# Performance work log

Measured on AMD Instinct MI355X. Metric: run time of the kernel, lower is better.

The kernel has to match this reference:

```python
import jax, jax.numpy as jnp
import numpy as np
from jax import lax

INPUT_SIZE = 64
HIDDEN = 64
LAYERS = 8
B, T = 256, 2048


def setup_inputs() -> dict:
    key = jax.random.key(0)
    ks = jax.random.split(key, 10)
    s = 1.0 / np.sqrt(HIDDEN)  # PyTorch RNN init scale U(-1/sqrt(h), 1/sqrt(h))
    u = lambda k, shape: jax.random.uniform(k, shape, jnp.float32, -s, s)
    return {
        "x": jax.random.normal(ks[0], (B, T, INPUT_SIZE), jnp.float32),
        "h_state": jnp.zeros((LAYERS, B, HIDDEN), jnp.float32),
        "W_ih0": u(ks[1], (HIDDEN, INPUT_SIZE)),        # layer-0 input weights
        "W_ih": u(ks[2], (LAYERS - 1, HIDDEN, HIDDEN)), # layers 1..7 input weights
        "W_hh": u(ks[3], (LAYERS, HIDDEN, HIDDEN)),
        "b_ih": u(ks[4], (LAYERS, HIDDEN)),
        "b_hh": u(ks[5], (LAYERS, HIDDEN)),
        "W_out": u(ks[6], (1, HIDDEN)),
        "b_out": u(ks[7], (1,)),
    }


def reference(x, h_state, W_ih0, W_ih, W_hh, b_ih, b_hh, W_out, b_out):
    # Precompute layer-0 input projection for all timesteps (one big GEMM).
    x_proj = jnp.einsum("bti,hi->bth", x, W_ih0) + b_ih[0]  # [B,T,H]
    xt = jnp.transpose(x_proj, (1, 0, 2))  # [T,B,H]

    def step(h, x_t):
        # h: [LAYERS, B, H]; one timestep of the 8-layer tanh RNN stack
        new_h = []
        inp = None
        for l in range(LAYERS):
            if l == 0:
                pre = x_t + h[0] @ W_hh[0].T + b_hh[0]
            else:
                pre = inp @ W_ih[l - 1].T + b_ih[l] + h[l] @ W_hh[l].T + b_hh[l]
            inp = jnp.tanh(pre)
            new_h.append(inp)
        return jnp.stack(new_h), inp  # carry, top-layer output

    h_final, tops = lax.scan(step, h_state, xt)  # tops: [T,B,H]
    # Batched output projection (replaces the per-timestep Python loop)
    y = jnp.transpose(tops @ W_out.T + b_out, (1, 0, 2))  # [B,T,1]
    return (y, h_final)
```

## Files before the change

kernel.cpp:

```cpp
#include <hip/hip_runtime.h>

typedef _Float16 h2 __attribute__((ext_vector_type(2)));
typedef _Float16 h8 __attribute__((ext_vector_type(8)));
typedef __fp16   g2 __attribute__((ext_vector_type(2)));
typedef __fp16   g8 __attribute__((ext_vector_type(8)));
typedef float    f32x4 __attribute__((ext_vector_type(4)));

#define TT 2048
#define HH 64
#define NL 8
#define NB 256
#define G  16
#define NCH (TT/G)
#define NI  (NCH + NL)

#define PRP 20
#define NNS 84

union GU { g8 v; g2 p[4]; h8 h; };

#define PH_BASE(l, P) (((l)*2 + (P)) * 2048)
#define CH_OFF(j, c)  ((j)*128 + ((((c) ^ ((j)&7))) * 16))

__device__ __forceinline__ float tanh_fast(float v){
    float e = __expf(2.0f * v);
    float r = __builtin_amdgcn_rcpf(e + 1.0f);
    return fmaf(-2.0f, r, 1.0f);
}


#define INTERVAL(MM, P, XC, XN) { \
    const int mm = (MM); \
    const bool act = (unsigned)(mm - wv) < (unsigned)NCH; \
    if (wv == 0){ \
        if (mm + 1 < NCH){ \
            _Pragma("unroll") \
            for (int j = 0; j < G; ++j) \
                *(_Float16*)(BB + PH_BASE(0, 1-(P)) + j*128 + (((lane>>3)^(j&7))*16) + (lane&7)*2) = (_Float16)XC[j]; \
        } \
        if (mm + 2 < NCH){ \
            _Pragma("unroll") \
            for (int j = 0; j < G; ++j) \
                XN[j] = x[((size_t)b*TT + (size_t)(mm+2)*G + j)*HH + lane]; \
        } \
    } \
    if (wv == 7 && mm >= 8){ \
         \
        GU ha0, ha1; \
        ha0.h = *(const h8*)(BB + PH_BASE(8, P) + CH_OFF(nn, g)); \
        ha1.h = *(const h8*)(BB + PH_BASE(8, P) + CH_OFF(nn, 4+g)); \
        f32x4 ay = {0.f, 0.f, 0.f, 0.f}; \
        ay = __builtin_amdgcn_mfma_f32_16x16x32_f16(ha0.v, woutB[0].v, ay, 0, 0, 0); \
        ay = __builtin_amdgcn_mfma_f32_16x16x32_f16(ha1.v, woutB[1].v, ay, 0, 0, 0); \
        if (nn == 0){ \
            f32x4 st; \
            st[0] = ay[0] + bout; st[1] = ay[1] + bout; \
            st[2] = ay[2] + bout; st[3] = ay[3] + bout; \
            *(f32x4*)(yout + (size_t)b*TT + (size_t)(mm-8)*G + g*4) = st; \
        } \
    } \
    if (act){ \
        if (wv > 0){ \
            while (((volatile int*)prodF)[wv] < mm) __builtin_amdgcn_s_sleep(1); \
            asm volatile("" ::: "memory"); \
        } \
         \
        GU bx0, bx1; \
        bx0.h = *(const h8*)(BB + PH_BASE(wv, P) + CH_OFF(nn, g)); \
        bx1.h = *(const h8*)(BB + PH_BASE(wv, P) + CH_OFF(nn, 4+g)); \
        f32x4 xd0 = {bs[0],bs[0],bs[0],bs[0]}, xd1 = {bs[1],bs[1],bs[1],bs[1]}; \
        f32x4 xd2 = {bs[2],bs[2],bs[2],bs[2]}, xd3 = {bs[3],bs[3],bs[3],bs[3]}; \
        xd0 = __builtin_amdgcn_mfma_f32_16x16x32_f16(bx0.v, wihA[0][0].v, xd0, 0, 0, 0); \
        xd0 = __builtin_amdgcn_mfma_f32_16x16x32_f16(bx1.v, wihA[0][1].v, xd0, 0, 0, 0); \
        xd1 = __builtin_amdgcn_mfma_f32_16x16x32_f16(bx0.v, wihA[1][0].v, xd1, 0, 0, 0); \
        xd1 = __builtin_amdgcn_mfma_f32_16x16x32_f16(bx1.v, wihA[1][1].v, xd1, 0, 0, 0); \
        xd2 = __builtin_amdgcn_mfma_f32_16x16x32_f16(bx0.v, wihA[2][0].v, xd2, 0, 0, 0); \
        xd2 = __builtin_amdgcn_mfma_f32_16x16x32_f16(bx1.v, wihA[2][1].v, xd2, 0, 0, 0); \
        xd3 = __builtin_amdgcn_mfma_f32_16x16x32_f16(bx0.v, wihA[3][0].v, xd3, 0, 0, 0); \
        xd3 = __builtin_amdgcn_mfma_f32_16x16x32_f16(bx1.v, wihA[3][1].v, xd3, 0, 0, 0); \
         \
        asm volatile("" ::: "memory"); \
        ((volatile int*)consF)[wv] = mm; \
         \
        *(f32x4*)(preTf + (size_t)(wv*16+nn)*NNS + 0*PRP + g*4) = xd0; \
        *(f32x4*)(preTf + (size_t)(wv*16+nn)*NNS + 1*PRP + g*4) = xd1; \
        *(f32x4*)(preTf + (size_t)(wv*16+nn)*NNS + 2*PRP + g*4) = xd2; \
        *(f32x4*)(preTf + (size_t)(wv*16+nn)*NNS + 3*PRP + g*4) = xd3; \
        f32x4 prv0, prv1, prv2, prv3; \
        { \
            const float* pb = preTf + (size_t)(wv*16+nn)*NNS + g*PRP; \
            prv0 = *(const f32x4*)(pb);      prv1 = *(const f32x4*)(pb + 4); \
            prv2 = *(const f32x4*)(pb + 8);  prv3 = *(const f32x4*)(pb + 12); \
        } \
         \
        if (wv < 7){ \
            while (((volatile int*)consF)[wv+1] < mm-1) __builtin_amdgcn_s_sleep(1); \
            asm volatile("" ::: "memory"); \
        } \
         \
        _Pragma("unroll") \
        for (int j = 0; j < G; ++j){ \
            GU hA0, hA1; \
            if (j == 0){ hA0 = hp0; hA1 = hp1; } \
            else { \
                hA0.h = *(const h8*)(BB + PH_BASE(wv+1, 1-(P)) + CH_OFF(j-1, g)); \
                hA1.h = *(const h8*)(BB + PH_BASE(wv+1, 1-(P)) + CH_OFF(j-1, 4+g)); \
            } \
            const f32x4 zz = {0.f, 0.f, 0.f, 0.f}; \
            f32x4 a00 = __builtin_amdgcn_mfma_f32_16x16x32_f16(hA0.v, whhB[0][0].v, zz, 0, 0, 0); \
            f32x4 a01 = __builtin_amdgcn_mfma_f32_16x16x32_f16(hA1.v, whhB[0][1].v, zz, 0, 0, 0); \
            f32x4 a10 = __builtin_amdgcn_mfma_f32_16x16x32_f16(hA0.v, whhB[1][0].v, zz, 0, 0, 0); \
            f32x4 a11 = __builtin_amdgcn_mfma_f32_16x16x32_f16(hA1.v, whhB[1][1].v, zz, 0, 0, 0); \
            f32x4 a20 = __builtin_amdgcn_mfma_f32_16x16x32_f16(hA0.v, whhB[2][0].v, zz, 0, 0, 0); \
            f32x4 a21 = __builtin_amdgcn_mfma_f32_16x16x32_f16(hA1.v, whhB[2][1].v, zz, 0, 0, 0); \
            f32x4 a30 = __builtin_amdgcn_mfma_f32_16x16x32_f16(hA0.v, whhB[3][0].v, zz, 0, 0, 0); \
            f32x4 a31 = __builtin_amdgcn_mfma_f32_16x16x32_f16(hA1.v, whhB[3][1].v, zz, 0, 0, 0); \
            const float s0 = a00[0] + a01[0], s1 = a10[0] + a11[0]; \
            const float s2 = a20[0] + a21[0], s3 = a30[0] + a31[0]; \
            const float pa = (g & 2) ? ((g & 1) ? s3 : s2) : ((g & 1) ? s1 : s0); \
            const float prj = (j < 4) ? prv0[j&3] : (j < 8) ? prv1[j&3] \
                             : (j < 12) ? prv2[j&3] : prv3[j&3]; \
            const float hn = tanh_fast(pa + prj); \
            *(_Float16*)(BB + PH_BASE(wv+1, 1-(P)) + j*128 + (((lane>>3)^(j&7))*16) + (lane&7)*2) = (_Float16)hn; \
            if (j == G-1){ \
                hp0.h = *(const h8*)(BB + PH_BASE(wv+1, 1-(P)) + CH_OFF(G-1, g)); \
                hp1.h = *(const h8*)(BB + PH_BASE(wv+1, 1-(P)) + CH_OFF(G-1, 4+g)); \
            } \
            if (mm - wv == NCH-1 && j == G-1) \
                hout[((size_t)wv*NB + b)*HH + lane] = hn; \
        } \
         \
        asm volatile("" ::: "memory"); \
        ((volatile int*)prodF)[wv+1] = mm + 1; \
    } \
}

__global__ void __launch_bounds__(512) rnn_kernel(
    const float* __restrict__ x,
    const float* __restrict__ h_state,
    const float* __restrict__ W_ih0,
    const float* __restrict__ W_ih,
    const float* __restrict__ W_hh,
    const float* __restrict__ b_ih,
    const float* __restrict__ b_hh,
    const float* __restrict__ W_out,
    const float* __restrict__ b_out,
    float* __restrict__ out)
{
    __shared__ __attribute__((aligned(16))) _Float16 buf[(NL+1)*2*G*HH];
    __shared__ __attribute__((aligned(16))) float preT[NL*16*NNS];
    __shared__ int prodF[16];
    __shared__ int consF[16];
    char* BB = (char*)buf;
    float* preTf = preT;
    const int tid  = threadIdx.x;
    const int wv   = tid >> 6;
    const int lane = tid & 63;
    const int g    = lane >> 4;
    const int nn   = lane & 15;
    const size_t b = blockIdx.x;

    GU wihA[4][2], whhB[4][2];
    const float* Wi = (wv == 0) ? W_ih0 : (W_ih + (size_t)(wv-1)*HH*HH);
    const float* Wh = W_hh + (size_t)wv*HH*HH;
    #pragma unroll
    for (int t = 0; t < 4; ++t){
        #pragma unroll
        for (int kt = 0; kt < 2; ++kt){
            const float* pi = Wi + (size_t)(t*16 + nn)*HH + kt*32 + g*8;
            const float* ph = Wh + (size_t)(t*16 + nn)*HH + kt*32 + g*8;
            f32x4 i0 = *(const f32x4*)(pi), i1 = *(const f32x4*)(pi + 4);
            f32x4 h0 = *(const f32x4*)(ph), h1 = *(const f32x4*)(ph + 4);
            wihA[t][kt].p[0] = __builtin_amdgcn_cvt_pkrtz(i0[0], i0[1]);
            wihA[t][kt].p[1] = __builtin_amdgcn_cvt_pkrtz(i0[2], i0[3]);
            wihA[t][kt].p[2] = __builtin_amdgcn_cvt_pkrtz(i1[0], i1[1]);
            wihA[t][kt].p[3] = __builtin_amdgcn_cvt_pkrtz(i1[2], i1[3]);
            whhB[t][kt].p[0] = __builtin_amdgcn_cvt_pkrtz(h0[0], h0[1]);
            whhB[t][kt].p[1] = __builtin_amdgcn_cvt_pkrtz(h0[2], h0[3]);
            whhB[t][kt].p[2] = __builtin_amdgcn_cvt_pkrtz(h1[0], h1[1]);
            whhB[t][kt].p[3] = __builtin_amdgcn_cvt_pkrtz(h1[2], h1[3]);
        }
    }
    float bs[4];
    #pragma unroll
    for (int t = 0; t < 4; ++t)
        bs[t] = b_ih[wv*HH + t*16 + nn] + b_hh[wv*HH + t*16 + nn];
    float bout = b_out[0];

    GU woutB[2];
    if (wv == 7){
        #pragma unroll
        for (int kt = 0; kt < 2; ++kt)
            #pragma unroll
            for (int q = 0; q < 4; ++q)
                woutB[kt].p[q] = __builtin_amdgcn_cvt_pkrtz(
                    W_out[kt*32 + g*8 + q*2], W_out[kt*32 + g*8 + q*2 + 1]);
    }

    for (int i = tid; i < (NL+1)*2*G*HH; i += 512) buf[i] = (_Float16)0.f;
    if (tid < 16){
        prodF[tid] = 0;
        consF[tid] = tid - 2;
    }
    __syncthreads();
    *(_Float16*)(BB + PH_BASE(wv+1, 1-(wv&1)) + (G-1)*128 + (((lane>>3)^((G-1)&7))*16) + (lane&7)*2)
        = (_Float16)h_state[((size_t)wv*NB + b)*HH + lane];
    float xa[G], xb[G];
    if (wv == 0){
        #pragma unroll
        for (int j = 0; j < G; ++j){
            *(_Float16*)(BB + PH_BASE(0, 1) + j*128 + (((lane>>3)^(j&7))*16) + (lane&7)*2)
                = (_Float16)x[((size_t)b*TT + j)*HH + lane];
            xa[j] = x[((size_t)b*TT + G + j)*HH + lane];
        }
    }
    __syncthreads();

    GU hp0, hp1;
    hp0.h = *(const h8*)(BB + PH_BASE(wv+1, 1-(wv&1)) + CH_OFF(G-1, g));
    hp1.h = *(const h8*)(BB + PH_BASE(wv+1, 1-(wv&1)) + CH_OFF(G-1, 4+g));

    float* yout = out;
    float* hout = out + (size_t)NB*TT;

    for (int m2 = 0; m2 < NI; m2 += 2){
        INTERVAL(m2,     1, xa, xb)
        INTERVAL(m2 + 1, 0, xb, xa)
    }
}

extern "C" void kernel_launch(void* const* d_in, const int* in_sizes, int n_in,
                              void* d_out, int out_size, void* d_ws, size_t ws_size,
                              hipStream_t stream) {
    (void)in_sizes; (void)n_in; (void)d_ws; (void)ws_size; (void)out_size;
    const float* x       = (const float*)d_in[0];
    const float* h_state = (const float*)d_in[1];
    const float* W_ih0   = (const float*)d_in[2];
    const float* W_ih    = (const float*)d_in[3];
    const float* W_hh    = (const float*)d_in[4];
    const float* b_ih    = (const float*)d_in[5];
    const float* b_hh    = (const float*)d_in[6];
    const float* W_out   = (const float*)d_in[7];
    const float* b_out   = (const float*)d_in[8];
    float* out = (float*)d_out;

    rnn_kernel<<<dim3(NB), dim3(512), 0, stream>>>(
        x, h_state, W_ih0, W_ih, W_hh, b_ih, b_hh, W_out, b_out, out);
}
```

Before: 479.9 us.

## Carry recurrent hidden state in registers via ds_bpermute instead of LDS round-trips

The serial recurrence inside each layer wave now keeps the new hidden state in packed registers and redistributes it to MFMA A-operand layout with ds_bpermute. This replaces the per-timestep LDS store-then-reload on the critical dependency chain. W_hh is reloaded in a permuted K order that matches the shuffled layout, and each lane now computes all four tanh outputs instead of selecting one. The precomputed input projections use a per-wave LDS area with a new stride and are loaded in quarters spread across the unrolled loop. The exchange costs more VALU work (four tanh per lane, eight bpermutes per step) and relies on the K-permutation being exactly consistent.

```diff
diff --git a/kernel.cpp b/kernel.cpp
--- a/kernel.cpp
+++ b/kernel.cpp
@@ -14,13 +14,15 @@
 #define NCH (TT/G)
 #define NI  (NCH + NL)
 
-#define PRP 20
-#define NNS 84
-
-union GU { g8 v; g2 p[4]; h8 h; };
+union GU  { g8 v; g2 p[4]; h8 h; };
+union FR8 { g8 v; int i[4]; };
+union IR  { int i; g2 h2v; };
 
 #define PH_BASE(l, P) (((l)*2 + (P)) * 2048)
 #define CH_OFF(j, c)  ((j)*128 + ((((c) ^ ((j)&7))) * 16))
+
+#define PRE_NN 68
+#define PRE_L  (16*PRE_NN)
 
 __device__ __forceinline__ float tanh_fast(float v){
     float e = __expf(2.0f * v);
@@ -28,6 +30,12 @@
     return fmaf(-2.0f, r, 1.0f);
 }
 
+
+#define LDQ(d0, d1, d2, d3, qd) { \
+    const float* pw = preW + nn*PRE_NN + (qd)*4; \
+    d0 = *(const f32x4*)(pw);      d1 = *(const f32x4*)(pw + 16); \
+    d2 = *(const f32x4*)(pw + 32); d3 = *(const f32x4*)(pw + 48); \
+}
 
 #define INTERVAL(MM, P, XC, XN) { \
     const int mm = (MM); \
@@ -45,7 +53,6 @@
         } \
     } \
     if (wv == 7 && mm >= 8){ \
-         \
         GU ha0, ha1; \
         ha0.h = *(const h8*)(BB + PH_BASE(8, P) + CH_OFF(nn, g)); \
         ha1.h = *(const h8*)(BB + PH_BASE(8, P) + CH_OFF(nn, 4+g)); \
@@ -78,58 +85,60 @@
         xd2 = __builtin_amdgcn_mfma_f32_16x16x32_f16(bx1.v, wihA[2][1].v, xd2, 0, 0, 0); \
         xd3 = __builtin_amdgcn_mfma_f32_16x16x32_f16(bx0.v, wihA[3][0].v, xd3, 0, 0, 0); \
         xd3 = __builtin_amdgcn_mfma_f32_16x16x32_f16(bx1.v, wihA[3][1].v, xd3, 0, 0, 0); \
-         \
         asm volatile("" ::: "memory"); \
         ((volatile int*)consF)[wv] = mm; \
          \
-        *(f32x4*)(preTf + (size_t)(wv*16+nn)*NNS + 0*PRP + g*4) = xd0; \
-        *(f32x4*)(preTf + (size_t)(wv*16+nn)*NNS + 1*PRP + g*4) = xd1; \
-        *(f32x4*)(preTf + (size_t)(wv*16+nn)*NNS + 2*PRP + g*4) = xd2; \
-        *(f32x4*)(preTf + (size_t)(wv*16+nn)*NNS + 3*PRP + g*4) = xd3; \
-        f32x4 prv0, prv1, prv2, prv3; \
-        { \
-            const float* pb = preTf + (size_t)(wv*16+nn)*NNS + g*PRP; \
-            prv0 = *(const f32x4*)(pb);      prv1 = *(const f32x4*)(pb + 4); \
-            prv2 = *(const f32x4*)(pb + 8);  prv3 = *(const f32x4*)(pb + 12); \
-        } \
-         \
+        *(f32x4*)(preW + nn*PRE_NN + 0*16 + gq) = xd0; \
+        *(f32x4*)(preW + nn*PRE_NN + 1*16 + gq) = xd1; \
+        *(f32x4*)(preW + nn*PRE_NN + 2*16 + gq) = xd2; \
+        *(f32x4*)(preW + nn*PRE_NN + 3*16 + gq) = xd3; \
         if (wv < 7){ \
             while (((volatile int*)consF)[wv+1] < mm-1) __builtin_amdgcn_s_sleep(1); \
             asm volatile("" ::: "memory"); \
         } \
+        f32x4 pA0, pA1, pA2, pA3, pB0, pB1, pB2, pB3; \
+        LDQ(pA0, pA1, pA2, pA3, 0) \
          \
         _Pragma("unroll") \
         for (int j = 0; j < G; ++j){ \
-            GU hA0, hA1; \
-            if (j == 0){ hA0 = hp0; hA1 = hp1; } \
-            else { \
-                hA0.h = *(const h8*)(BB + PH_BASE(wv+1, 1-(P)) + CH_OFF(j-1, g)); \
-                hA1.h = *(const h8*)(BB + PH_BASE(wv+1, 1-(P)) + CH_OFF(j-1, 4+g)); \
-            } \
+            FR8 hf0, hf1; \
+            hf0.i[0] = __builtin_amdgcn_ds_bpermute(bpa0, P0i); \
+            hf0.i[1] = __builtin_amdgcn_ds_bpermute(bpa1, P0i); \
+            hf0.i[2] = __builtin_amdgcn_ds_bpermute(bpa2, P0i); \
+            hf0.i[3] = __builtin_amdgcn_ds_bpermute(bpa3, P0i); \
+            hf1.i[0] = __builtin_amdgcn_ds_bpermute(bpa0, P1i); \
+            hf1.i[1] = __builtin_amdgcn_ds_bpermute(bpa1, P1i); \
+            hf1.i[2] = __builtin_amdgcn_ds_bpermute(bpa2, P1i); \
+            hf1.i[3] = __builtin_amdgcn_ds_bpermute(bpa3, P1i); \
             const f32x4 zz = {0.f, 0.f, 0.f, 0.f}; \
-            f32x4 a00 = __builtin_amdgcn_mfma_f32_16x16x32_f16(hA0.v, whhB[0][0].v, zz, 0, 0, 0); \
-            f32x4 a01 = __builtin_amdgcn_mfma_f32_16x16x32_f16(hA1.v, whhB[0][1].v, zz, 0, 0, 0); \
-            f32x4 a10 = __builtin_amdgcn_mfma_f32_16x16x32_f16(hA0.v, whhB[1][0].v, zz, 0, 0, 0); \
-            f32x4 a11 = __builtin_amdgcn_mfma_f32_16x16x32_f16(hA1.v, whhB[1][1].v, zz, 0, 0, 0); \
-            f32x4 a20 = __builtin_amdgcn_mfma_f32_16x16x32_f16(hA0.v, whhB[2][0].v, zz, 0, 0, 0); \
-            f32x4 a21 = __builtin_amdgcn_mfma_f32_16x16x32_f16(hA1.v, whhB[2][1].v, zz, 0, 0, 0); \
-            f32x4 a30 = __builtin_amdgcn_mfma_f32_16x16x32_f16(hA0.v, whhB[3][0].v, zz, 0, 0, 0); \
-            f32x4 a31 = __builtin_amdgcn_mfma_f32_16x16x32_f16(hA1.v, whhB[3][1].v, zz, 0, 0, 0); \
-            const float s0 = a00[0] + a01[0], s1 = a10[0] + a11[0]; \
-            const float s2 = a20[0] + a21[0], s3 = a30[0] + a31[0]; \
-            const float pa = (g & 2) ? ((g & 1) ? s3 : s2) : ((g & 1) ? s1 : s0); \
-            const float prj = (j < 4) ? prv0[j&3] : (j < 8) ? prv1[j&3] \
-                             : (j < 12) ? prv2[j&3] : prv3[j&3]; \
-            const float hn = tanh_fast(pa + prj); \
-            *(_Float16*)(BB + PH_BASE(wv+1, 1-(P)) + j*128 + (((lane>>3)^(j&7))*16) + (lane&7)*2) = (_Float16)hn; \
-            if (j == G-1){ \
-                hp0.h = *(const h8*)(BB + PH_BASE(wv+1, 1-(P)) + CH_OFF(G-1, g)); \
-                hp1.h = *(const h8*)(BB + PH_BASE(wv+1, 1-(P)) + CH_OFF(G-1, 4+g)); \
-            } \
+            f32x4 a00 = __builtin_amdgcn_mfma_f32_16x16x32_f16(hf0.v, whhB2[0][0].v, zz, 0, 0, 0); \
+            f32x4 a01 = __builtin_amdgcn_mfma_f32_16x16x32_f16(hf1.v, whhB2[0][1].v, zz, 0, 0, 0); \
+            f32x4 a10 = __builtin_amdgcn_mfma_f32_16x16x32_f16(hf0.v, whhB2[1][0].v, zz, 0, 0, 0); \
+            f32x4 a11 = __builtin_amdgcn_mfma_f32_16x16x32_f16(hf1.v, whhB2[1][1].v, zz, 0, 0, 0); \
+            f32x4 a20 = __builtin_amdgcn_mfma_f32_16x16x32_f16(hf0.v, whhB2[2][0].v, zz, 0, 0, 0); \
+            f32x4 a21 = __builtin_amdgcn_mfma_f32_16x16x32_f16(hf1.v, whhB2[2][1].v, zz, 0, 0, 0); \
+            f32x4 a30 = __builtin_amdgcn_mfma_f32_16x16x32_f16(hf0.v, whhB2[3][0].v, zz, 0, 0, 0); \
+            f32x4 a31 = __builtin_amdgcn_mfma_f32_16x16x32_f16(hf1.v, whhB2[3][1].v, zz, 0, 0, 0); \
+            float p0, p1, p2, p3; \
+            if (j < 4)      { p0 = pA0[j&3]; p1 = pA1[j&3]; p2 = pA2[j&3]; p3 = pA3[j&3]; } \
+            else if (j < 8) { p0 = pB0[j&3]; p1 = pB1[j&3]; p2 = pB2[j&3]; p3 = pB3[j&3]; } \
+            else if (j < 12){ p0 = pA0[j&3]; p1 = pA1[j&3]; p2 = pA2[j&3]; p3 = pA3[j&3]; } \
+            else            { p0 = pB0[j&3]; p1 = pB1[j&3]; p2 = pB2[j&3]; p3 = pB3[j&3]; } \
+            const float th0 = tanh_fast(a00[0] + a01[0] + p0); \
+            const float th1 = tanh_fast(a10[0] + a11[0] + p1); \
+            const float th2 = tanh_fast(a20[0] + a21[0] + p2); \
+            const float th3 = tanh_fast(a30[0] + a31[0] + p3); \
+            IR n0, n1; \
+            n0.h2v = __builtin_amdgcn_cvt_pkrtz(th0, th1); P0i = n0.i; \
+            n1.h2v = __builtin_amdgcn_cvt_pkrtz(th2, th3); P1i = n1.i; \
+            const float hsel = (g & 2) ? ((g & 1) ? th3 : th2) : ((g & 1) ? th1 : th0); \
+            *(_Float16*)(BB + PH_BASE(wv+1, 1-(P)) + j*128 + (((lane>>3)^(j&7))*16) + (lane&7)*2) = (_Float16)hsel; \
+            if (j == 1)  LDQ(pB0, pB1, pB2, pB3, 1) \
+            if (j == 5)  LDQ(pA0, pA1, pA2, pA3, 2) \
+            if (j == 9)  LDQ(pB0, pB1, pB2, pB3, 3) \
             if (mm - wv == NCH-1 && j == G-1) \
-                hout[((size_t)wv*NB + b)*HH + lane] = hn; \
-        } \
-         \
+                hout[((size_t)wv*NB + b)*HH + lane] = hsel; \
+        } \
         asm volatile("" ::: "memory"); \
         ((volatile int*)prodF)[wv+1] = mm + 1; \
     } \
@@ -148,37 +157,51 @@
     float* __restrict__ out)
 {
     __shared__ __attribute__((aligned(16))) _Float16 buf[(NL+1)*2*G*HH];
-    __shared__ __attribute__((aligned(16))) float preT[NL*16*NNS];
+    __shared__ __attribute__((aligned(16))) float preT2[NL*PRE_L];
     __shared__ int prodF[16];
     __shared__ int consF[16];
     char* BB = (char*)buf;
-    float* preTf = preT;
     const int tid  = threadIdx.x;
     const int wv   = tid >> 6;
     const int lane = tid & 63;
     const int g    = lane >> 4;
     const int nn   = lane & 15;
+    const int gq   = g*4;
     const size_t b = blockIdx.x;
-
-    GU wihA[4][2], whhB[4][2];
+    float* preW = preT2 + wv*PRE_L;
+
+    const int bpa0 = ((lane & 32) | (gq + 0)) << 2;
+    const int bpa1 = ((lane & 32) | (gq + 1)) << 2;
+    const int bpa2 = ((lane & 32) | (gq + 2)) << 2;
+    const int bpa3 = ((lane & 32) | (gq + 3)) << 2;
+
+    GU wihA[4][2];
     const float* Wi = (wv == 0) ? W_ih0 : (W_ih + (size_t)(wv-1)*HH*HH);
-    const float* Wh = W_hh + (size_t)wv*HH*HH;
     #pragma unroll
     for (int t = 0; t < 4; ++t){
         #pragma unroll
         for (int kt = 0; kt < 2; ++kt){
             const float* pi = Wi + (size_t)(t*16 + nn)*HH + kt*32 + g*8;
-            const float* ph = Wh + (size_t)(t*16 + nn)*HH + kt*32 + g*8;
             f32x4 i0 = *(const f32x4*)(pi), i1 = *(const f32x4*)(pi + 4);
-            f32x4 h0 = *(const f32x4*)(ph), h1 = *(const f32x4*)(ph + 4);
             wihA[t][kt].p[0] = __builtin_amdgcn_cvt_pkrtz(i0[0], i0[1]);
             wihA[t][kt].p[1] = __builtin_amdgcn_cvt_pkrtz(i0[2], i0[3]);
             wihA[t][kt].p[2] = __builtin_amdgcn_cvt_pkrtz(i1[0], i1[1]);
             wihA[t][kt].p[3] = __builtin_amdgcn_cvt_pkrtz(i1[2], i1[3]);
-            whhB[t][kt].p[0] = __builtin_amdgcn_cvt_pkrtz(h0[0], h0[1]);
-            whhB[t][kt].p[1] = __builtin_amdgcn_cvt_pkrtz(h0[2], h0[3]);
-            whhB[t][kt].p[2] = __builtin_amdgcn_cvt_pkrtz(h1[0], h1[1]);
-            whhB[t][kt].p[3] = __builtin_amdgcn_cvt_pkrtz(h1[2], h1[3]);
+        }
+    }
+    GU whhB2[4][2];
+    const float* Wh = W_hh + (size_t)wv*HH*HH;
+    #pragma unroll
+    for (int t = 0; t < 4; ++t){
+        #pragma unroll
+        for (int kt = 0; kt < 2; ++kt){
+            const float* ph = Wh + (size_t)(t*16 + nn)*HH + kt*32;
+            f32x4 c0 = *(const f32x4*)(ph + gq);
+            f32x4 c1 = *(const f32x4*)(ph + 16 + gq);
+            whhB2[t][kt].p[0] = __builtin_amdgcn_cvt_pkrtz(c0[0], c1[0]);
+            whhB2[t][kt].p[1] = __builtin_amdgcn_cvt_pkrtz(c0[1], c1[1]);
+            whhB2[t][kt].p[2] = __builtin_amdgcn_cvt_pkrtz(c0[2], c1[2]);
+            whhB2[t][kt].p[3] = __builtin_amdgcn_cvt_pkrtz(c0[3], c1[3]);
         }
     }
     float bs[4];
@@ -197,14 +220,20 @@
                     W_out[kt*32 + g*8 + q*2], W_out[kt*32 + g*8 + q*2 + 1]);
     }
 
+    int P0i, P1i;
+    {
+        const float* hsb = h_state + ((size_t)wv*NB + b)*HH + nn;
+        IR u0, u1;
+        u0.h2v = __builtin_amdgcn_cvt_pkrtz(hsb[0],  hsb[16]); P0i = u0.i;
+        u1.h2v = __builtin_amdgcn_cvt_pkrtz(hsb[32], hsb[48]); P1i = u1.i;
+    }
+
     for (int i = tid; i < (NL+1)*2*G*HH; i += 512) buf[i] = (_Float16)0.f;
     if (tid < 16){
         prodF[tid] = 0;
         consF[tid] = tid - 2;
     }
     __syncthreads();
-    *(_Float16*)(BB + PH_BASE(wv+1, 1-(wv&1)) + (G-1)*128 + (((lane>>3)^((G-1)&7))*16) + (lane&7)*2)
-        = (_Float16)h_state[((size_t)wv*NB + b)*HH + lane];
     float xa[G], xb[G];
     if (wv == 0){
         #pragma unroll
@@ -215,10 +244,6 @@
         }
     }
     __syncthreads();
-
-    GU hp0, hp1;
-    hp0.h = *(const h8*)(BB + PH_BASE(wv+1, 1-(wv&1)) + CH_OFF(G-1, g));
-    hp1.h = *(const h8*)(BB + PH_BASE(wv+1, 1-(wv&1)) + CH_OFF(G-1, 4+g));
 
     float* yout = out;
     float* hout = out + (size_t)NB*TT;
```

After: 689.9 us. 1.44x slower.

## Process two batch rows per block and stream x via global_load_lds

Applied to the files above, without the earlier changes.

Each workgroup now handles two batch elements, so the grid is halved and each wave interleaves two independent recurrences per timestep to hide MFMA and tanh latency. Layer-0 input is loaded directly into LDS with global_load_lds double buffering and converted on read, replacing the register staging by wave 0. The pre-activation buffer layout changes to per-batch, per-layer rows, and waves-per-EU is pinned. This roughly doubles LDS use and per-wave work, and uses only 128 blocks, which may underfill the device's CUs.

```diff
diff --git a/kernel.cpp b/kernel.cpp
--- a/kernel.cpp
+++ b/kernel.cpp
@@ -10,17 +10,22 @@
 #define HH 64
 #define NL 8
 #define NB 256
+#define NBT 2
+#define NGRID (NB/NBT)
 #define G  16
 #define NCH (TT/G)
 #define NI  (NCH + NL)
 
-#define PRP 20
-#define NNS 84
-
-union GU { g8 v; g2 p[4]; h8 h; };
-
-#define PH_BASE(l, P) (((l)*2 + (P)) * 2048)
+union GU  { g8 v; g2 p[4]; h8 h; };
+
+#define BUFB(bt, idx, P) ((((bt)*8 + (idx))*2 + (P)) * 2048)
 #define CH_OFF(j, c)  ((j)*128 + ((((c) ^ ((j)&7))) * 16))
+
+#define PRE_ROW 68
+#define PRE_LYR (16*PRE_ROW)
+#define XQ_ROW 68
+#define XQ_PH  (16*XQ_ROW)
+#define XQ_BT  (2*XQ_PH)
 
 __device__ __forceinline__ float tanh_fast(float v){
     float e = __expf(2.0f * v);
@@ -28,35 +33,113 @@
     return fmaf(-2.0f, r, 1.0f);
 }
 
-
-#define INTERVAL(MM, P, XC, XN) { \
+__device__ __forceinline__ void gload_lds4(const float* g, float* l){
+    __builtin_amdgcn_global_load_lds(
+        (const __attribute__((address_space(1))) void*)g,
+        (__attribute__((address_space(3))) void*)l, 4, 0, 0);
+}
+
+
+#define XPROJ(bx0_, bx1_, preb) { \
+    f32x4 x0 = {bs[0],bs[0],bs[0],bs[0]}, x1 = {bs[1],bs[1],bs[1],bs[1]}; \
+    f32x4 x2 = {bs[2],bs[2],bs[2],bs[2]}, x3 = {bs[3],bs[3],bs[3],bs[3]}; \
+    x0 = __builtin_amdgcn_mfma_f32_16x16x32_f16(bx0_.v, wihA[0][0].v, x0, 0, 0, 0); \
+    x0 = __builtin_amdgcn_mfma_f32_16x16x32_f16(bx1_.v, wihA[0][1].v, x0, 0, 0, 0); \
+    x1 = __builtin_amdgcn_mfma_f32_16x16x32_f16(bx0_.v, wihA[1][0].v, x1, 0, 0, 0); \
+    x1 = __builtin_amdgcn_mfma_f32_16x16x32_f16(bx1_.v, wihA[1][1].v, x1, 0, 0, 0); \
+    x2 = __builtin_amdgcn_mfma_f32_16x16x32_f16(bx0_.v, wihA[2][0].v, x2, 0, 0, 0); \
+    x2 = __builtin_amdgcn_mfma_f32_16x16x32_f16(bx1_.v, wihA[2][1].v, x2, 0, 0, 0); \
+    x3 = __builtin_amdgcn_mfma_f32_16x16x32_f16(bx0_.v, wihA[3][0].v, x3, 0, 0, 0); \
+    x3 = __builtin_amdgcn_mfma_f32_16x16x32_f16(bx1_.v, wihA[3][1].v, x3, 0, 0, 0); \
+    *(f32x4*)((preb) + nn*PRE_ROW + 0*16 + gq) = x0; \
+    *(f32x4*)((preb) + nn*PRE_ROW + 1*16 + gq) = x1; \
+    *(f32x4*)((preb) + nn*PRE_ROW + 2*16 + gq) = x2; \
+    *(f32x4*)((preb) + nn*PRE_ROW + 3*16 + gq) = x3; \
+}
+
+#define XQREAD(bx0_, bx1_, xrp) { \
+    f32x4 q0 = *(const f32x4*)((xrp) + g*8); \
+    f32x4 q1 = *(const f32x4*)((xrp) + g*8 + 4); \
+    f32x4 q2 = *(const f32x4*)((xrp) + 32 + g*8); \
+    f32x4 q3 = *(const f32x4*)((xrp) + 36 + g*8); \
+    bx0_.p[0] = __builtin_amdgcn_cvt_pkrtz(q0[0], q0[1]); \
+    bx0_.p[1] = __builtin_amdgcn_cvt_pkrtz(q0[2], q0[3]); \
+    bx0_.p[2] = __builtin_amdgcn_cvt_pkrtz(q1[0], q1[1]); \
+    bx0_.p[3] = __builtin_amdgcn_cvt_pkrtz(q1[2], q1[3]); \
+    bx1_.p[0] = __builtin_amdgcn_cvt_pkrtz(q2[0], q2[1]); \
+    bx1_.p[1] = __builtin_amdgcn_cvt_pkrtz(q2[2], q2[3]); \
+    bx1_.p[2] = __builtin_amdgcn_cvt_pkrtz(q3[0], q3[1]); \
+    bx1_.p[3] = __builtin_amdgcn_cvt_pkrtz(q3[2], q3[3]); \
+}
+
+#define DO_STEP2(jj, PW, mm_) { \
+    GU hA0, hA1, hB0, hB1; \
+    if ((jj) == 0){ hA0 = hpA0; hA1 = hpA1; hB0 = hpB0; hB1 = hpB1; } \
+    else { \
+        hA0.h = *(const h8*)(BB + BUFB(0, wv, PW) + CH_OFF((jj)-1, g)); \
+        hA1.h = *(const h8*)(BB + BUFB(0, wv, PW) + CH_OFF((jj)-1, 4+g)); \
+        hB0.h = *(const h8*)(BB + BUFB(1, wv, PW) + CH_OFF((jj)-1, g)); \
+        hB1.h = *(const h8*)(BB + BUFB(1, wv, PW) + CH_OFF((jj)-1, 4+g)); \
+    } \
+    const float prA = preA[nn*PRE_ROW + g*16 + (jj)]; \
+    const float prB = preB[nn*PRE_ROW + g*16 + (jj)]; \
+    const f32x4 zz = {0.f, 0.f, 0.f, 0.f}; \
+    f32x4 aA0 = __builtin_amdgcn_mfma_f32_16x16x32_f16(hA0.v, whhB[0][0].v, zz, 0, 0, 0); \
+    f32x4 aA1 = __builtin_amdgcn_mfma_f32_16x16x32_f16(hA0.v, whhB[1][0].v, zz, 0, 0, 0); \
+    f32x4 aA2 = __builtin_amdgcn_mfma_f32_16x16x32_f16(hA0.v, whhB[2][0].v, zz, 0, 0, 0); \
+    f32x4 aA3 = __builtin_amdgcn_mfma_f32_16x16x32_f16(hA0.v, whhB[3][0].v, zz, 0, 0, 0); \
+    f32x4 aB0 = __builtin_amdgcn_mfma_f32_16x16x32_f16(hB0.v, whhB[0][0].v, zz, 0, 0, 0); \
+    f32x4 aB1 = __builtin_amdgcn_mfma_f32_16x16x32_f16(hB0.v, whhB[1][0].v, zz, 0, 0, 0); \
+    f32x4 aB2 = __builtin_amdgcn_mfma_f32_16x16x32_f16(hB0.v, whhB[2][0].v, zz, 0, 0, 0); \
+    f32x4 aB3 = __builtin_amdgcn_mfma_f32_16x16x32_f16(hB0.v, whhB[3][0].v, zz, 0, 0, 0); \
+    aA0 = __builtin_amdgcn_mfma_f32_16x16x32_f16(hA1.v, whhB[0][1].v, aA0, 0, 0, 0); \
+    aA1 = __builtin_amdgcn_mfma_f32_16x16x32_f16(hA1.v, whhB[1][1].v, aA1, 0, 0, 0); \
+    aA2 = __builtin_amdgcn_mfma_f32_16x16x32_f16(hA1.v, whhB[2][1].v, aA2, 0, 0, 0); \
+    aA3 = __builtin_amdgcn_mfma_f32_16x16x32_f16(hA1.v, whhB[3][1].v, aA3, 0, 0, 0); \
+    aB0 = __builtin_amdgcn_mfma_f32_16x16x32_f16(hB1.v, whhB[0][1].v, aB0, 0, 0, 0); \
+    aB1 = __builtin_amdgcn_mfma_f32_16x16x32_f16(hB1.v, whhB[1][1].v, aB1, 0, 0, 0); \
+    aB2 = __builtin_amdgcn_mfma_f32_16x16x32_f16(hB1.v, whhB[2][1].v, aB2, 0, 0, 0); \
+    aB3 = __builtin_amdgcn_mfma_f32_16x16x32_f16(hB1.v, whhB[3][1].v, aB3, 0, 0, 0); \
+    const float tA01 = (g & 1) ? aA1[0] : aA0[0]; \
+    const float tA23 = (g & 1) ? aA3[0] : aA2[0]; \
+    const float hnA  = tanh_fast(((g & 2) ? tA23 : tA01) + prA); \
+    const float tB01 = (g & 1) ? aB1[0] : aB0[0]; \
+    const float tB23 = (g & 1) ? aB3[0] : aB2[0]; \
+    const float hnB  = tanh_fast(((g & 2) ? tB23 : tB01) + prB); \
+    *(_Float16*)(BB + BUFB(0, wv, PW) + (jj)*128 + (((lane>>3)^((jj)&7))*16) + (lane&7)*2) = (_Float16)hnA; \
+    *(_Float16*)(BB + BUFB(1, wv, PW) + (jj)*128 + (((lane>>3)^((jj)&7))*16) + (lane&7)*2) = (_Float16)hnB; \
+    if ((jj) == G-1){ \
+        hpA0.h = *(const h8*)(BB + BUFB(0, wv, PW) + CH_OFF(G-1, g)); \
+        hpA1.h = *(const h8*)(BB + BUFB(0, wv, PW) + CH_OFF(G-1, 4+g)); \
+        hpB0.h = *(const h8*)(BB + BUFB(1, wv, PW) + CH_OFF(G-1, g)); \
+        hpB1.h = *(const h8*)(BB + BUFB(1, wv, PW) + CH_OFF(G-1, 4+g)); \
+        if ((mm_) - wv == NCH-1){ \
+            hout[((size_t)wv*NB + b0)*HH + lane] = hnA; \
+            hout[((size_t)wv*NB + b1)*HH + lane] = hnB; \
+        } \
+    } \
+}
+
+#define INTERVAL(MM, P) { \
     const int mm = (MM); \
     const bool act = (unsigned)(mm - wv) < (unsigned)NCH; \
-    if (wv == 0){ \
-        if (mm + 1 < NCH){ \
-            _Pragma("unroll") \
-            for (int j = 0; j < G; ++j) \
-                *(_Float16*)(BB + PH_BASE(0, 1-(P)) + j*128 + (((lane>>3)^(j&7))*16) + (lane&7)*2) = (_Float16)XC[j]; \
-        } \
-        if (mm + 2 < NCH){ \
-            _Pragma("unroll") \
-            for (int j = 0; j < G; ++j) \
-                XN[j] = x[((size_t)b*TT + (size_t)(mm+2)*G + j)*HH + lane]; \
-        } \
-    } \
     if (wv == 7 && mm >= 8){ \
-         \
-        GU ha0, ha1; \
-        ha0.h = *(const h8*)(BB + PH_BASE(8, P) + CH_OFF(nn, g)); \
-        ha1.h = *(const h8*)(BB + PH_BASE(8, P) + CH_OFF(nn, 4+g)); \
-        f32x4 ay = {0.f, 0.f, 0.f, 0.f}; \
-        ay = __builtin_amdgcn_mfma_f32_16x16x32_f16(ha0.v, woutB[0].v, ay, 0, 0, 0); \
-        ay = __builtin_amdgcn_mfma_f32_16x16x32_f16(ha1.v, woutB[1].v, ay, 0, 0, 0); \
+        GU ya0, ya1, yb0, yb1; \
+        ya0.h = *(const h8*)(BB + BUFB(0, 7, P) + CH_OFF(nn, g)); \
+        ya1.h = *(const h8*)(BB + BUFB(0, 7, P) + CH_OFF(nn, 4+g)); \
+        yb0.h = *(const h8*)(BB + BUFB(1, 7, P) + CH_OFF(nn, g)); \
+        yb1.h = *(const h8*)(BB + BUFB(1, 7, P) + CH_OFF(nn, 4+g)); \
+        f32x4 ayA = {0.f,0.f,0.f,0.f}, ayB = {0.f,0.f,0.f,0.f}; \
+        ayA = __builtin_amdgcn_mfma_f32_16x16x32_f16(ya0.v, woutB[0].v, ayA, 0, 0, 0); \
+        ayA = __builtin_amdgcn_mfma_f32_16x16x32_f16(ya1.v, woutB[1].v, ayA, 0, 0, 0); \
+        ayB = __builtin_amdgcn_mfma_f32_16x16x32_f16(yb0.v, woutB[0].v, ayB, 0, 0, 0); \
+        ayB = __builtin_amdgcn_mfma_f32_16x16x32_f16(yb1.v, woutB[1].v, ayB, 0, 0, 0); \
         if (nn == 0){ \
-            f32x4 st; \
-            st[0] = ay[0] + bout; st[1] = ay[1] + bout; \
-            st[2] = ay[2] + bout; st[3] = ay[3] + bout; \
-            *(f32x4*)(yout + (size_t)b*TT + (size_t)(mm-8)*G + g*4) = st; \
+            f32x4 sA, sB; \
+            sA[0]=ayA[0]+bout; sA[1]=ayA[1]+bout; sA[2]=ayA[2]+bout; sA[3]=ayA[3]+bout; \
+            sB[0]=ayB[0]+bout; sB[1]=ayB[1]+bout; sB[2]=ayB[2]+bout; sB[3]=ayB[3]+bout; \
+            *(f32x4*)(yout + (size_t)b0*TT + (size_t)(mm-8)*G + g*4) = sA; \
+            *(f32x4*)(yout + (size_t)b1*TT + (size_t)(mm-8)*G + g*4) = sB; \
         } \
     } \
     if (act){ \
@@ -64,77 +147,46 @@
             while (((volatile int*)prodF)[wv] < mm) __builtin_amdgcn_s_sleep(1); \
             asm volatile("" ::: "memory"); \
         } \
-         \
-        GU bx0, bx1; \
-        bx0.h = *(const h8*)(BB + PH_BASE(wv, P) + CH_OFF(nn, g)); \
-        bx1.h = *(const h8*)(BB + PH_BASE(wv, P) + CH_OFF(nn, 4+g)); \
-        f32x4 xd0 = {bs[0],bs[0],bs[0],bs[0]}, xd1 = {bs[1],bs[1],bs[1],bs[1]}; \
-        f32x4 xd2 = {bs[2],bs[2],bs[2],bs[2]}, xd3 = {bs[3],bs[3],bs[3],bs[3]}; \
-        xd0 = __builtin_amdgcn_mfma_f32_16x16x32_f16(bx0.v, wihA[0][0].v, xd0, 0, 0, 0); \
-        xd0 = __builtin_amdgcn_mfma_f32_16x16x32_f16(bx1.v, wihA[0][1].v, xd0, 0, 0, 0); \
-        xd1 = __builtin_amdgcn_mfma_f32_16x16x32_f16(bx0.v, wihA[1][0].v, xd1, 0, 0, 0); \
-        xd1 = __builtin_amdgcn_mfma_f32_16x16x32_f16(bx1.v, wihA[1][1].v, xd1, 0, 0, 0); \
-        xd2 = __builtin_amdgcn_mfma_f32_16x16x32_f16(bx0.v, wihA[2][0].v, xd2, 0, 0, 0); \
-        xd2 = __builtin_amdgcn_mfma_f32_16x16x32_f16(bx1.v, wihA[2][1].v, xd2, 0, 0, 0); \
-        xd3 = __builtin_amdgcn_mfma_f32_16x16x32_f16(bx0.v, wihA[3][0].v, xd3, 0, 0, 0); \
-        xd3 = __builtin_amdgcn_mfma_f32_16x16x32_f16(bx1.v, wihA[3][1].v, xd3, 0, 0, 0); \
-         \
+        GU bxA0, bxA1, bxB0, bxB1; \
+        if (wv == 0){ \
+            asm volatile("s_waitcnt vmcnt(0)" ::: "memory"); \
+            XQREAD(bxA0, bxA1, xqA + (mm&1)*XQ_PH + nn*XQ_ROW) \
+            XQREAD(bxB0, bxB1, xqB + (mm&1)*XQ_PH + nn*XQ_ROW) \
+            if (mm + 1 < NCH){ \
+                const float* gx0 = x + ((size_t)b0*TT + (size_t)(mm+1)*G)*HH + lane; \
+                const float* gx1 = x + ((size_t)b1*TT + (size_t)(mm+1)*G)*HH + lane; \
+                float* lq0 = xqA + (1-(mm&1))*XQ_PH; \
+                float* lq1 = xqB + (1-(mm&1))*XQ_PH; \
+                _Pragma("unroll") \
+                for (int j = 0; j < G; ++j){ \
+                    gload_lds4(gx0 + j*HH, lq0 + j*XQ_ROW); \
+                    gload_lds4(gx1 + j*HH, lq1 + j*XQ_ROW); \
+                } \
+            } \
+        } else { \
+            bxA0.h = *(const h8*)(BB + BUFB(0, wv-1, P) + CH_OFF(nn, g)); \
+            bxA1.h = *(const h8*)(BB + BUFB(0, wv-1, P) + CH_OFF(nn, 4+g)); \
+            bxB0.h = *(const h8*)(BB + BUFB(1, wv-1, P) + CH_OFF(nn, g)); \
+            bxB1.h = *(const h8*)(BB + BUFB(1, wv-1, P) + CH_OFF(nn, 4+g)); \
+        } \
+        XPROJ(bxA0, bxA1, preA) \
+        XPROJ(bxB0, bxB1, preB) \
         asm volatile("" ::: "memory"); \
         ((volatile int*)consF)[wv] = mm; \
-         \
-        *(f32x4*)(preTf + (size_t)(wv*16+nn)*NNS + 0*PRP + g*4) = xd0; \
-        *(f32x4*)(preTf + (size_t)(wv*16+nn)*NNS + 1*PRP + g*4) = xd1; \
-        *(f32x4*)(preTf + (size_t)(wv*16+nn)*NNS + 2*PRP + g*4) = xd2; \
-        *(f32x4*)(preTf + (size_t)(wv*16+nn)*NNS + 3*PRP + g*4) = xd3; \
-        f32x4 prv0, prv1, prv2, prv3; \
-        { \
-            const float* pb = preTf + (size_t)(wv*16+nn)*NNS + g*PRP; \
-            prv0 = *(const f32x4*)(pb);      prv1 = *(const f32x4*)(pb + 4); \
-            prv2 = *(const f32x4*)(pb + 8);  prv3 = *(const f32x4*)(pb + 12); \
-        } \
-         \
         if (wv < 7){ \
             while (((volatile int*)consF)[wv+1] < mm-1) __builtin_amdgcn_s_sleep(1); \
             asm volatile("" ::: "memory"); \
         } \
-         \
         _Pragma("unroll") \
         for (int j = 0; j < G; ++j){ \
-            GU hA0, hA1; \
-            if (j == 0){ hA0 = hp0; hA1 = hp1; } \
-            else { \
-                hA0.h = *(const h8*)(BB + PH_BASE(wv+1, 1-(P)) + CH_OFF(j-1, g)); \
-                hA1.h = *(const h8*)(BB + PH_BASE(wv+1, 1-(P)) + CH_OFF(j-1, 4+g)); \
-            } \
-            const f32x4 zz = {0.f, 0.f, 0.f, 0.f}; \
-            f32x4 a00 = __builtin_amdgcn_mfma_f32_16x16x32_f16(hA0.v, whhB[0][0].v, zz, 0, 0, 0); \
-            f32x4 a01 = __builtin_amdgcn_mfma_f32_16x16x32_f16(hA1.v, whhB[0][1].v, zz, 0, 0, 0); \
-            f32x4 a10 = __builtin_amdgcn_mfma_f32_16x16x32_f16(hA0.v, whhB[1][0].v, zz, 0, 0, 0); \
-            f32x4 a11 = __builtin_amdgcn_mfma_f32_16x16x32_f16(hA1.v, whhB[1][1].v, zz, 0, 0, 0); \
-            f32x4 a20 = __builtin_amdgcn_mfma_f32_16x16x32_f16(hA0.v, whhB[2][0].v, zz, 0, 0, 0); \
-            f32x4 a21 = __builtin_amdgcn_mfma_f32_16x16x32_f16(hA1.v, whhB[2][1].v, zz, 0, 0, 0); \
-            f32x4 a30 = __builtin_amdgcn_mfma_f32_16x16x32_f16(hA0.v, whhB[3][0].v, zz, 0, 0, 0); \
-            f32x4 a31 = __builtin_amdgcn_mfma_f32_16x16x32_f16(hA1.v, whhB[3][1].v, zz, 0, 0, 0); \
-            const float s0 = a00[0] + a01[0], s1 = a10[0] + a11[0]; \
-            const float s2 = a20[0] + a21[0], s3 = a30[0] + a31[0]; \
-            const float pa = (g & 2) ? ((g & 1) ? s3 : s2) : ((g & 1) ? s1 : s0); \
-            const float prj = (j < 4) ? prv0[j&3] : (j < 8) ? prv1[j&3] \
-                             : (j < 12) ? prv2[j&3] : prv3[j&3]; \
-            const float hn = tanh_fast(pa + prj); \
-            *(_Float16*)(BB + PH_BASE(wv+1, 1-(P)) + j*128 + (((lane>>3)^(j&7))*16) + (lane&7)*2) = (_Float16)hn; \
-            if (j == G-1){ \
-                hp0.h = *(const h8*)(BB + PH_BASE(wv+1, 1-(P)) + CH_OFF(G-1, g)); \
-                hp1.h = *(const h8*)(BB + PH_BASE(wv+1, 1-(P)) + CH_OFF(G-1, 4+g)); \
-            } \
-            if (mm - wv == NCH-1 && j == G-1) \
-                hout[((size_t)wv*NB + b)*HH + lane] = hn; \
-        } \
-         \
+            DO_STEP2(j, 1-(P), mm) \
+        } \
         asm volatile("" ::: "memory"); \
         ((volatile int*)prodF)[wv+1] = mm + 1; \
     } \
 }
 
+__attribute__((amdgpu_waves_per_eu(2, 2)))
 __global__ void __launch_bounds__(512) rnn_kernel(
     const float* __restrict__ x,
     const float* __restrict__ h_state,
@@ -147,18 +199,24 @@
     const float* __restrict__ b_out,
     float* __restrict__ out)
 {
-    __shared__ __attribute__((aligned(16))) _Float16 buf[(NL+1)*2*G*HH];
-    __shared__ __attribute__((aligned(16))) float preT[NL*16*NNS];
+    __shared__ __attribute__((aligned(16))) _Float16 buf[NBT*8*2*16*64];
+    __shared__ __attribute__((aligned(16))) float pre[NBT*NL*PRE_LYR];
+    __shared__ __attribute__((aligned(16))) float xq[NBT*XQ_BT];
     __shared__ int prodF[16];
     __shared__ int consF[16];
     char* BB = (char*)buf;
-    float* preTf = preT;
     const int tid  = threadIdx.x;
     const int wv   = tid >> 6;
     const int lane = tid & 63;
     const int g    = lane >> 4;
     const int nn   = lane & 15;
-    const size_t b = blockIdx.x;
+    const int gq   = g*4;
+    const size_t b0 = (size_t)blockIdx.x * NBT;
+    const size_t b1 = b0 + 1;
+    float* preA = pre + (size_t)(0*NL + wv)*PRE_LYR;
+    float* preB = pre + (size_t)(1*NL + wv)*PRE_LYR;
+    float* xqA  = xq;
+    float* xqB  = xq + XQ_BT;
 
     GU wihA[4][2], whhB[4][2];
     const float* Wi = (wv == 0) ? W_ih0 : (W_ih + (size_t)(wv-1)*HH*HH);
@@ -197,35 +255,39 @@
                     W_out[kt*32 + g*8 + q*2], W_out[kt*32 + g*8 + q*2 + 1]);
     }
 
-    for (int i = tid; i < (NL+1)*2*G*HH; i += 512) buf[i] = (_Float16)0.f;
+    for (int i = tid; i < NBT*8*2*16*64; i += 512) buf[i] = (_Float16)0.f;
     if (tid < 16){
         prodF[tid] = 0;
         consF[tid] = tid - 2;
     }
     __syncthreads();
-    *(_Float16*)(BB + PH_BASE(wv+1, 1-(wv&1)) + (G-1)*128 + (((lane>>3)^((G-1)&7))*16) + (lane&7)*2)
-        = (_Float16)h_state[((size_t)wv*NB + b)*HH + lane];
-    float xa[G], xb[G];
+    *(_Float16*)(BB + BUFB(0, wv, 1-(wv&1)) + (G-1)*128 + (((lane>>3)^((G-1)&7))*16) + (lane&7)*2)
+        = (_Float16)h_state[((size_t)wv*NB + b0)*HH + lane];
+    *(_Float16*)(BB + BUFB(1, wv, 1-(wv&1)) + (G-1)*128 + (((lane>>3)^((G-1)&7))*16) + (lane&7)*2)
+        = (_Float16)h_state[((size_t)wv*NB + b1)*HH + lane];
     if (wv == 0){
+        const float* gx0 = x + (size_t)b0*TT*HH + lane;
+        const float* gx1 = x + (size_t)b1*TT*HH + lane;
         #pragma unroll
         for (int j = 0; j < G; ++j){
-            *(_Float16*)(BB + PH_BASE(0, 1) + j*128 + (((lane>>3)^(j&7))*16) + (lane&7)*2)
-                = (_Float16)x[((size_t)b*TT + j)*HH + lane];
-            xa[j] = x[((size_t)b*TT + G + j)*HH + lane];
+            gload_lds4(gx0 + j*HH, xqA + j*XQ_ROW);
+            gload_lds4(gx1 + j*HH, xqB + j*XQ_ROW);
         }
     }
     __syncthreads();
 
-    GU hp0, hp1;
-    hp0.h = *(const h8*)(BB + PH_BASE(wv+1, 1-(wv&1)) + CH_OFF(G-1, g));
-    hp1.h = *(const h8*)(BB + PH_BASE(wv+1, 1-(wv&1)) + CH_OFF(G-1, 4+g));
+    GU hpA0, hpA1, hpB0, hpB1;
+    hpA0.h = *(const h8*)(BB + BUFB(0, wv, 1-(wv&1)) + CH_OFF(G-1, g));
+    hpA1.h = *(const h8*)(BB + BUFB(0, wv, 1-(wv&1)) + CH_OFF(G-1, 4+g));
+    hpB0.h = *(const h8*)(BB + BUFB(1, wv, 1-(wv&1)) + CH_OFF(G-1, g));
+    hpB1.h = *(const h8*)(BB + BUFB(1, wv, 1-(wv&1)) + CH_OFF(G-1, 4+g));
 
     float* yout = out;
     float* hout = out + (size_t)NB*TT;
 
     for (int m2 = 0; m2 < NI; m2 += 2){
-        INTERVAL(m2,     1, xa, xb)
-        INTERVAL(m2 + 1, 0, xb, xa)
+        INTERVAL(m2,     1)
+        INTERVAL(m2 + 1, 0)
     }
 }
 
@@ -244,6 +306,6 @@
     const float* b_out   = (const float*)d_in[8];
     float* out = (float*)d_out;
 
-    rnn_kernel<<<dim3(NB), dim3(512), 0, stream>>>(
+    rnn_kernel<<<dim3(NGRID), dim3(512), 0, stream>>>(
         x, h_state, W_ih0, W_ih, W_hh, b_ih, b_hh, W_out, b_out, out);
 }
```

Result: slower. 753.8 us (+57.1%).
